# Kernel optimization log

Measured on AMD Instinct MI355X. Metric: run time of the kernel, lower is better.

The kernel has to match this reference:

```python
import jax, jax.numpy as jnp
import numpy as np

B, S, D, H, DH = 2, 2048, 1024, 16, 64
EPS = 1e-6


def setup_inputs() -> dict:
    key = jax.random.key(0)
    k0, k1, k2 = jax.random.split(key, 3)
    x = jax.random.normal(k0, (B, S, D), dtype=jnp.float32)
    mask = jnp.ones((B, S), dtype=bool)
    # NeoX-style rotary angles: half-dim inverse freqs, duplicated to rot_dim=DH
    inv_freq = 1.0 / (10000.0 ** (jnp.arange(0, DH, 2, dtype=jnp.float32) / DH))  # [DH/2]
    ang = jnp.arange(S, dtype=jnp.float32)[:, None] * inv_freq[None, :]            # [S, DH/2]
    freqs = jnp.concatenate([ang, ang], axis=-1)                                    # [S, DH]
    W_qkv = jax.random.normal(k1, (3 * D, D), dtype=jnp.float32) * (D ** -0.5)
    W_out = jax.random.normal(k2, (D, D), dtype=jnp.float32) * (D ** -0.5)
    q_gamma = jnp.ones((DH,), jnp.float32)
    q_beta = jnp.zeros((DH,), jnp.float32)
    k_gamma = jnp.ones((DH,), jnp.float32)
    k_beta = jnp.zeros((DH,), jnp.float32)
    return {"x": x, "mask": mask, "freqs": freqs, "W_qkv": W_qkv, "W_out": W_out,
            "q_gamma": q_gamma, "q_beta": q_beta, "k_gamma": k_gamma, "k_beta": k_beta}


def _layernorm(t, g, b):
    mu = t.mean(-1, keepdims=True)
    var = t.var(-1, keepdims=True)
    return (t - mu) * jax.lax.rsqrt(var + EPS) * g + b


def _rotate_half(t):
    t1, t2 = jnp.split(t, 2, axis=-1)
    return jnp.concatenate([-t2, t1], axis=-1)


def reference(x, mask, freqs, W_qkv, W_out, q_gamma, q_beta, k_gamma, k_beta):
    b, s, d = x.shape
    # fused QKV projection + split into heads: b n (h d) -> b h n d
    qkv = x @ W_qkv.T                                   # [b, s, 3d]
    q, k, v = jnp.split(qkv, 3, axis=-1)
    to_heads = lambda t: t.reshape(b, s, H, DH).transpose(0, 2, 1, 3)
    q, k, v = to_heads(q), to_heads(k), to_heads(v)      # [b, h, s, dh]
    # qk layernorm
    q = _layernorm(q, q_gamma, q_beta)
    k = _layernorm(k, k_gamma, k_beta)
    # rotary embedding (fp32 path in the original; inputs already fp32)
    cos = jnp.cos(freqs)[None, None]                      # [1, 1, s, dh]
    sin = jnp.sin(freqs)[None, None]
    q = q * cos + _rotate_half(q) * sin
    k = k * cos + _rotate_half(k) * sin
    # mask construction: key padding mask 'b j -> b 1 1 j' combined with causal
    key_mask = mask[:, None, None, :]                     # [b, 1, 1, s]
    causal = jnp.tril(jnp.ones((s, s), dtype=bool))       # [s, s]
    comb = key_mask & causal[None, None]                  # [b, 1, s, s]
    row_masked = ~comb.any(axis=-1)                       # [b, 1, s]
    comb = comb.at[..., 0].set(comb[..., 0] | row_masked)
    # SDPA
    scale = DH ** -0.5
    scores = jnp.einsum('bhid,bhjd->bhij', q, k) * scale  # [b, h, s, s]
    scores = jnp.where(comb, scores, jnp.finfo(scores.dtype).min)
    attn = jax.nn.softmax(scores, axis=-1)
    out = jnp.einsum('bhij,bhjd->bhid', attn, v)          # [b, h, s, dh]
    out = jnp.where(row_masked[..., None], 0.0, out)
    # merge heads + output projection
    out = out.transpose(0, 2, 1, 3).reshape(b, s, d)
    return out @ W_out.T
```

## Files before the change

### kernel.cpp

```cpp
#include <hip/hip_runtime.h>
#include <hip/hip_bf16.h>
#include <cstdint>

typedef unsigned short u16;
typedef __attribute__((ext_vector_type(8))) short s16x8;
typedef __attribute__((ext_vector_type(4))) float f32x4;
typedef __attribute__((ext_vector_type(16))) float f32x16;
typedef __attribute__((ext_vector_type(4))) unsigned int u32x4;
typedef __attribute__((ext_vector_type(2))) unsigned int u32x2;
typedef __attribute__((ext_vector_type(4))) u16 u16x4;

#define LOG2E 1.44269504088896340736f

__device__ __forceinline__ u16 f2b(float f) {
  union { float f; unsigned u; } v; v.f = f;
  unsigned r = v.u + 0x7FFF + ((v.u >> 16) & 1);
  return (u16)(r >> 16);
}

__device__ __forceinline__ void gload_lds16(const u16* g, u16* l) {
  __builtin_amdgcn_global_load_lds((const __attribute__((address_space(1))) void*)g,
                                   (__attribute__((address_space(3))) void*)l, 16, 0, 0);
}

__global__ void cvt_bf16(const float* __restrict__ in, u16* __restrict__ out, int n) {
  int i = blockIdx.x * blockDim.x + threadIdx.x;
  if (i < n) out[i] = f2b(in[i]);
}

__global__ void trig_tab(const float* __restrict__ f, float* __restrict__ c,
                         float* __restrict__ s, int n) {
  int i = blockIdx.x * blockDim.x + threadIdx.x;
  if (i < n) { c[i] = cosf(f[i]); s[i] = sinf(f[i]); }
}

__global__ __launch_bounds__(256) void gemm_bt(const u16* __restrict__ A, const u16* __restrict__ B,
                                               float* __restrict__ C, int M, int N, int K) {
  __shared__ u16 sA[128 * 64];
  __shared__ u16 sB[128 * 64];
  const int nbn = N >> 7;
  int bx = blockIdx.x % nbn, by = blockIdx.x / nbn;
  int tid = threadIdx.x, w = tid >> 6, lane = tid & 63;
  int wr = (w >> 1) * 64, wc = (w & 1) * 64;
  int lr = lane >> 3, lc = lane & 7;
  f32x4 acc[4][4] = {};
  size_t arow = (size_t)(by * 128) * K;
  size_t brow = (size_t)(bx * 128) * K;
  for (int k0 = 0; k0 < K; k0 += 64) {
    __syncthreads();
    for (int c = 0; c < 4; ++c) {
      int r = w * 32 + c * 8;
      gload_lds16(A + arow + (size_t)(r + lr) * K + k0 + lc * 8, &sA[r * 64]);
      gload_lds16(B + brow + (size_t)(r + lr) * K + k0 + lc * 8, &sB[r * 64]);
    }
    __syncthreads();
    for (int kk = 0; kk < 64; kk += 32) {
      s16x8 af[4], bf[4];
      int ro = lane & 15, ko = kk + (lane >> 4) * 8;
      for (int m = 0; m < 4; ++m) af[m] = *(const s16x8*)&sA[(wr + m * 16 + ro) * 64 + ko];
      for (int n = 0; n < 4; ++n) bf[n] = *(const s16x8*)&sB[(wc + n * 16 + ro) * 64 + ko];
      for (int m = 0; m < 4; ++m)
        for (int n = 0; n < 4; ++n)
          acc[m][n] = __builtin_amdgcn_mfma_f32_16x16x32_bf16(af[m], bf[n], acc[m][n], 0, 0, 0);
    }
  }
  int ro = lane & 15, rg = lane >> 4;
  for (int m = 0; m < 4; ++m)
    for (int n = 0; n < 4; ++n) {
      int row = by * 128 + wr + m * 16 + rg * 4;
      int col = bx * 128 + wc + n * 16 + ro;
      float* cp = C + (size_t)row * N + col;
      for (int r = 0; r < 4; ++r) cp[(size_t)r * N] = acc[m][n][r];
    }
}

__global__ __launch_bounds__(256) void ln_rope(const float* __restrict__ qkv,
    const float* __restrict__ cosT, const float* __restrict__ sinT,
    const float* __restrict__ qg, const float* __restrict__ qb,
    const float* __restrict__ kg, const float* __restrict__ kb,
    u16* __restrict__ qo, u16* __restrict__ ko, u16* __restrict__ vo) {
  int gw = (blockIdx.x * 256 + threadIdx.x) >> 6;
  int lane = threadIdx.x & 63;
  int h = gw & 15, bs = gw >> 4;
  int s = bs & 2047, b = bs >> 11;
  const float* row = qkv + (size_t)bs * 3072;
  float qv = row[h * 64 + lane];
  float kv = row[1024 + h * 64 + lane];
  float vv = row[2048 + h * 64 + lane];

  float s1q = qv, s2q = qv * qv, s1k = kv, s2k = kv * kv;
  for (int off = 1; off < 64; off <<= 1) {
    s1q += __shfl_xor(s1q, off, 64); s2q += __shfl_xor(s2q, off, 64);
    s1k += __shfl_xor(s1k, off, 64); s2k += __shfl_xor(s2k, off, 64);
  }
  float muq = s1q * (1.f / 64.f), varq = s2q * (1.f / 64.f) - muq * muq;
  float muk = s1k * (1.f / 64.f), vark = s2k * (1.f / 64.f) - muk * muk;
  float qn = (qv - muq) * rsqrtf(varq + 1e-6f) * qg[lane] + qb[lane];
  float kn = (kv - muk) * rsqrtf(vark + 1e-6f) * kg[lane] + kb[lane];

  float cs = cosT[s * 64 + lane], sn = sinT[s * 64 + lane];
  float qh = __shfl_xor(qn, 32, 64); qh = (lane < 32) ? -qh : qh;
  float kh = __shfl_xor(kn, 32, 64); kh = (lane < 32) ? -kh : kh;
  float qr = (qn * cs + qh * sn) * 0.125f;
  float kr = kn * cs + kh * sn;

  size_t oidx = ((size_t)((b * 16 + h) * 2048 + s)) * 64 + lane;
  qo[oidx] = f2b(qr); ko[oidx] = f2b(kr); vo[oidx] = f2b(vv);
}

__global__ __launch_bounds__(256) void transpose_v(const u16* __restrict__ vi, u16* __restrict__ vt) {
  __shared__ __align__(16) u16 tile[64][72];
  int bh = blockIdx.x >> 5, st = blockIdx.x & 31;
  int t = threadIdx.x;
  const u16* src = vi + ((size_t)bh * 2048 + st * 64) * 64;
  int r = t & 63, c = (t >> 6) * 16;
  *(s16x8*)&tile[r][c]     = *(const s16x8*)(src + r * 64 + c);
  *(s16x8*)&tile[r][c + 8] = *(const s16x8*)(src + r * 64 + c + 8);
  __syncthreads();
  int dh = t & 63, so = (t >> 6) * 16;
  alignas(16) u16 buf[16];
  #pragma unroll
  for (int j = 0; j < 16; ++j) buf[j] = tile[so + j][dh];
  u16* dst = vt + ((size_t)bh * 64 + dh) * 2048 + st * 64 + so;
  *(s16x8*)dst       = *(const s16x8*)&buf[0];
  *(s16x8*)(dst + 8) = *(const s16x8*)&buf[8];
}

__global__ __launch_bounds__(64) void attn_fwd2(const u16* __restrict__ qp, const u16* __restrict__ kp,
                                                const u16* __restrict__ vtp, u16* __restrict__ op) {
  __shared__ __align__(16) u16 ot[32][72];
  int bid = ((blockIdx.x & 7) << 7) | (blockIdx.x >> 3);
  int bh = bid >> 5, pr = bid & 31;
  int l = threadIdx.x;
  int ql = l & 31, h5 = l >> 5;
  int b = bh >> 4, h = bh & 15;
  const u16* qb = qp + (size_t)bh * 2048 * 64;
  const u16* kb = kp + (size_t)bh * 2048 * 64;
  const u16* vb = vtp + (size_t)bh * 64 * 2048;

  for (int ss = 0; ss < 2; ++ss) {
    int strip = ss ? (63 - pr) : pr;
    int q0 = strip * 32;
    s16x8 qf[4];
    {
      const u16* qr = qb + (size_t)(q0 + ql) * 64 + h5 * 8;
      #pragma unroll
      for (int t = 0; t < 4; ++t) qf[t] = *(const s16x8*)(qr + 16 * t);
    }
    f32x16 o0 = {}, o1 = {};
    float m = -INFINITY, lsum = 0.f;

    for (int kt = 0; kt <= strip; ++kt) {
      const u16* kr = kb + (size_t)(kt * 32 + ql) * 64 + h5 * 8;
      s16x8 kf[4];
      #pragma unroll
      for (int t = 0; t < 4; ++t) kf[t] = *(const s16x8*)(kr + 16 * t);
      const u16* vr = vb + (size_t)ql * 2048 + kt * 32 + h5 * 8;
      s16x8 vf00 = *(const s16x8*)(vr);
      s16x8 vf01 = *(const s16x8*)(vr + 16);
      s16x8 vf10 = *(const s16x8*)(vr + 32 * 2048);
      s16x8 vf11 = *(const s16x8*)(vr + 32 * 2048 + 16);

      f32x16 sc = {};
      #pragma unroll
      for (int t = 0; t < 4; ++t)
        sc = __builtin_amdgcn_mfma_f32_32x32x16_bf16(kf[t], qf[t], sc, 0, 0, 0);

      if (kt == strip) {
        #pragma unroll
        for (int r = 0; r < 16; ++r) {
          int kloc = (r & 3) + 8 * (r >> 2) + 4 * h5;
          sc[r] = (kloc > ql) ? -INFINITY : sc[r];
        }
      }
      float mx = sc[0];
      #pragma unroll
      for (int r = 1; r < 16; ++r) mx = fmaxf(mx, sc[r]);
      mx = fmaxf(mx, __shfl_xor(mx, 32, 64));
      float mn = fmaxf(m, mx);
      float alpha = __builtin_amdgcn_exp2f((m - mn) * LOG2E);
      float rs = 0.f;
      #pragma unroll
      for (int r = 0; r < 16; ++r) {
        float p = __builtin_amdgcn_exp2f((sc[r] - mn) * LOG2E);
        sc[r] = p; rs += p;
      }
      rs += __shfl_xor(rs, 32, 64);
      lsum = lsum * alpha + rs;
      m = mn;
      #pragma unroll
      for (int r = 0; r < 16; ++r) { o0[r] *= alpha; o1[r] *= alpha; }

      unsigned w[8];
      #pragma unroll
      for (int i = 0; i < 8; ++i)
        asm("v_cvt_pk_bf16_f32 %0, %1, %2" : "=v"(w[i]) : "v"(sc[2 * i]), "v"(sc[2 * i + 1]));
      u32x2 r02 = __builtin_amdgcn_permlane32_swap(w[0], w[2], false, false);
      u32x2 r13 = __builtin_amdgcn_permlane32_swap(w[1], w[3], false, false);
      u32x2 r46 = __builtin_amdgcn_permlane32_swap(w[4], w[6], false, false);
      u32x2 r57 = __builtin_amdgcn_permlane32_swap(w[5], w[7], false, false);
      u32x4 t0v = {r02[0], r13[0], r02[1], r13[1]};
      u32x4 t1v = {r46[0], r57[0], r46[1], r57[1]};
      s16x8 pa0 = __builtin_bit_cast(s16x8, t0v);
      s16x8 pa1 = __builtin_bit_cast(s16x8, t1v);

      o0 = __builtin_amdgcn_mfma_f32_32x32x16_bf16(vf00, pa0, o0, 0, 0, 0);
      o0 = __builtin_amdgcn_mfma_f32_32x32x16_bf16(vf01, pa1, o0, 0, 0, 0);
      o1 = __builtin_amdgcn_mfma_f32_32x32x16_bf16(vf10, pa0, o1, 0, 0, 0);
      o1 = __builtin_amdgcn_mfma_f32_32x32x16_bf16(vf11, pa1, o1, 0, 0, 0);
    }

    float invl = 1.f / lsum;
    #pragma unroll
    for (int d = 0; d < 2; ++d) {
      #pragma unroll
      for (int g = 0; g < 4; ++g) {
        const f32x16& o = d ? o1 : o0;
        u16x4 pkv = { f2b(o[g * 4 + 0] * invl), f2b(o[g * 4 + 1] * invl),
                      f2b(o[g * 4 + 2] * invl), f2b(o[g * 4 + 3] * invl) };
        *(u16x4*)&ot[ql][d * 32 + g * 8 + h5 * 4] = pkv;
      }
    }
    __syncthreads();
    {
      int qrow = l >> 1, dh0 = (l & 1) * 32;
      u16* dst = op + ((size_t)(b * 2048 + q0 + qrow)) * 1024 + h * 64 + dh0;
      #pragma unroll
      for (int k = 0; k < 4; ++k)
        *(s16x8*)(dst + 8 * k) = *(const s16x8*)&ot[qrow][dh0 + 8 * k];
    }
    __syncthreads();
  }
}

extern "C" void kernel_launch(void* const* d_in, const int* in_sizes, int n_in,
                              void* d_out, int out_size, void* d_ws, size_t ws_size,
                              hipStream_t stream) {
  const float* x     = (const float*)d_in[0];
  const float* freqs = (const float*)d_in[2];
  const float* Wqkv  = (const float*)d_in[3];
  const float* Wout  = (const float*)d_in[4];
  const float* qg    = (const float*)d_in[5];
  const float* qb    = (const float*)d_in[6];
  const float* kg    = (const float*)d_in[7];
  const float* kb    = (const float*)d_in[8];
  float* out = (float*)d_out;

  u16* xb    = (u16*)d_ws;
  u16* wqkvb = xb + 4194304;
  u16* woutb = wqkvb + 3145728;
  float* cosT = (float*)(woutb + 1048576);
  float* sinT = cosT + 131072;
  float* qkv  = sinT + 131072;
  u16* qo = (u16*)(qkv + 12582912);
  u16* ko = qo + 4194304;
  u16* vo = ko + 4194304;
  u16* ao = vo + 4194304;
  u16* vt = (u16*)qkv;

  cvt_bf16<<<(4194304 + 255) / 256, 256, 0, stream>>>(x, xb, 4194304);
  cvt_bf16<<<(3145728 + 255) / 256, 256, 0, stream>>>(Wqkv, wqkvb, 3145728);
  cvt_bf16<<<(1048576 + 255) / 256, 256, 0, stream>>>(Wout, woutb, 1048576);
  trig_tab<<<(131072 + 255) / 256, 256, 0, stream>>>(freqs, cosT, sinT, 131072);

  gemm_bt<<<(4096 / 128) * (3072 / 128), 256, 0, stream>>>(xb, wqkvb, qkv, 4096, 3072, 1024);
  ln_rope<<<65536 / 4, 256, 0, stream>>>(qkv, cosT, sinT, qg, qb, kg, kb, qo, ko, vo);
  transpose_v<<<32 * 32, 256, 0, stream>>>(vo, vt);
  attn_fwd2<<<32 * 32, 64, 0, stream>>>(qo, ko, vt, ao);
  gemm_bt<<<(4096 / 128) * (1024 / 128), 256, 0, stream>>>(ao, woutb, out, 4096, 1024, 1024);
}
```

Baseline: 273.9 us.

## Split attention strips into separate blocks, double-buffer K loads, skip redundant rescales

The attention kernel now launches one 64-thread block per 32-row query strip, 2048 blocks in total, where before each block handled two paired strips. Block-to-(head, strip) mapping is derived from the XCD index so each XCD works on a fixed set of heads, which should improve L2 reuse of K/V. K fragments for the next tile are prefetched into alternating register sets while the current tile computes. The row-max reduction becomes a tree, and the alpha rescale of the accumulators is skipped when no lane's max increased. The cost is more blocks with smaller, uneven work per block and higher register pressure from the double-buffered K.

```diff
diff --git a/kernel.cpp b/kernel.cpp
--- a/kernel.cpp
+++ b/kernel.cpp
@@ -126,110 +126,130 @@
   *(s16x8*)(dst + 8) = *(const s16x8*)&buf[8];
 }
 
-__global__ __launch_bounds__(64) void attn_fwd2(const u16* __restrict__ qp, const u16* __restrict__ kp,
+#define LDK(R0, R1, R2, R3, KT) do { \
+    const u16* kr_ = kptr + (size_t)((KT) * 32 + ql) * 64 + h5 * 8; \
+    R0 = *(const s16x8*)(kr_);      R1 = *(const s16x8*)(kr_ + 16); \
+    R2 = *(const s16x8*)(kr_ + 32); R3 = *(const s16x8*)(kr_ + 48); \
+  } while (0)
+
+__global__ __launch_bounds__(64) void attn_fwd3(const u16* __restrict__ qp, const u16* __restrict__ kp,
                                                 const u16* __restrict__ vtp, u16* __restrict__ op) {
   __shared__ __align__(16) u16 ot[32][72];
-  int bid = ((blockIdx.x & 7) << 7) | (blockIdx.x >> 3);
-  int bh = bid >> 5, pr = bid & 31;
+  int bid = blockIdx.x;
+  int xcd = bid & 7, rr = bid >> 3, k8 = rr >> 5, cu = rr & 31;
+  int bh = 4 * xcd + (k8 & 3);
+  int strip = (k8 >> 2) ? (63 - cu) : cu;
   int l = threadIdx.x;
   int ql = l & 31, h5 = l >> 5;
   int b = bh >> 4, h = bh & 15;
-  const u16* qb = qp + (size_t)bh * 2048 * 64;
-  const u16* kb = kp + (size_t)bh * 2048 * 64;
-  const u16* vb = vtp + (size_t)bh * 64 * 2048;
-
-  for (int ss = 0; ss < 2; ++ss) {
-    int strip = ss ? (63 - pr) : pr;
-    int q0 = strip * 32;
-    s16x8 qf[4];
-    {
-      const u16* qr = qb + (size_t)(q0 + ql) * 64 + h5 * 8;
+  const u16* qptr = qp + (size_t)bh * 2048 * 64;
+  const u16* kptr = kp + (size_t)bh * 2048 * 64;
+  const u16* vptr = vtp + (size_t)bh * 64 * 2048;
+
+  int q0 = strip * 32;
+  s16x8 qf[4];
+  {
+    const u16* qr = qptr + (size_t)(q0 + ql) * 64 + h5 * 8;
+    #pragma unroll
+    for (int t = 0; t < 4; ++t) qf[t] = *(const s16x8*)(qr + 16 * t);
+  }
+  f32x16 o0 = {}, o1 = {};
+  float m = -INFINITY, lsum = 0.f;
+
+  auto tile = [&](s16x8 k0, s16x8 k1, s16x8 k2, s16x8 k3, int kt) {
+    const u16* vr = vptr + (size_t)ql * 2048 + kt * 32 + h5 * 8;
+    s16x8 v00 = *(const s16x8*)(vr);
+    s16x8 v01 = *(const s16x8*)(vr + 16);
+    s16x8 v10 = *(const s16x8*)(vr + 32 * 2048);
+    s16x8 v11 = *(const s16x8*)(vr + 32 * 2048 + 16);
+
+    f32x16 sc = {};
+    sc = __builtin_amdgcn_mfma_f32_32x32x16_bf16(k0, qf[0], sc, 0, 0, 0);
+    sc = __builtin_amdgcn_mfma_f32_32x32x16_bf16(k1, qf[1], sc, 0, 0, 0);
+    sc = __builtin_amdgcn_mfma_f32_32x32x16_bf16(k2, qf[2], sc, 0, 0, 0);
+    sc = __builtin_amdgcn_mfma_f32_32x32x16_bf16(k3, qf[3], sc, 0, 0, 0);
+
+    if (kt == strip) {
       #pragma unroll
-      for (int t = 0; t < 4; ++t) qf[t] = *(const s16x8*)(qr + 16 * t);
-    }
-    f32x16 o0 = {}, o1 = {};
-    float m = -INFINITY, lsum = 0.f;
-
-    for (int kt = 0; kt <= strip; ++kt) {
-      const u16* kr = kb + (size_t)(kt * 32 + ql) * 64 + h5 * 8;
-      s16x8 kf[4];
-      #pragma unroll
-      for (int t = 0; t < 4; ++t) kf[t] = *(const s16x8*)(kr + 16 * t);
-      const u16* vr = vb + (size_t)ql * 2048 + kt * 32 + h5 * 8;
-      s16x8 vf00 = *(const s16x8*)(vr);
-      s16x8 vf01 = *(const s16x8*)(vr + 16);
-      s16x8 vf10 = *(const s16x8*)(vr + 32 * 2048);
-      s16x8 vf11 = *(const s16x8*)(vr + 32 * 2048 + 16);
-
-      f32x16 sc = {};
-      #pragma unroll
-      for (int t = 0; t < 4; ++t)
-        sc = __builtin_amdgcn_mfma_f32_32x32x16_bf16(kf[t], qf[t], sc, 0, 0, 0);
-
-      if (kt == strip) {
-        #pragma unroll
-        for (int r = 0; r < 16; ++r) {
-          int kloc = (r & 3) + 8 * (r >> 2) + 4 * h5;
-          sc[r] = (kloc > ql) ? -INFINITY : sc[r];
-        }
+      for (int r = 0; r < 16; ++r) {
+        int kloc = (r & 3) + 8 * (r >> 2) + 4 * h5;
+        sc[r] = (kloc > ql) ? -INFINITY : sc[r];
       }
-      float mx = sc[0];
-      #pragma unroll
-      for (int r = 1; r < 16; ++r) mx = fmaxf(mx, sc[r]);
-      mx = fmaxf(mx, __shfl_xor(mx, 32, 64));
+    }
+    float t8[8], t4[4];
+    #pragma unroll
+    for (int i = 0; i < 8; ++i) t8[i] = fmaxf(sc[2 * i], sc[2 * i + 1]);
+    #pragma unroll
+    for (int i = 0; i < 4; ++i) t4[i] = fmaxf(t8[2 * i], t8[2 * i + 1]);
+    float mx = fmaxf(fmaxf(t4[0], t4[1]), fmaxf(t4[2], t4[3]));
+    mx = fmaxf(mx, __shfl_xor(mx, 32, 64));
+
+    if (__any(mx > m)) {
       float mn = fmaxf(m, mx);
       float alpha = __builtin_amdgcn_exp2f((m - mn) * LOG2E);
-      float rs = 0.f;
-      #pragma unroll
-      for (int r = 0; r < 16; ++r) {
-        float p = __builtin_amdgcn_exp2f((sc[r] - mn) * LOG2E);
-        sc[r] = p; rs += p;
-      }
-      rs += __shfl_xor(rs, 32, 64);
-      lsum = lsum * alpha + rs;
-      m = mn;
       #pragma unroll
       for (int r = 0; r < 16; ++r) { o0[r] *= alpha; o1[r] *= alpha; }
-
-      unsigned w[8];
-      #pragma unroll
-      for (int i = 0; i < 8; ++i)
-        asm("v_cvt_pk_bf16_f32 %0, %1, %2" : "=v"(w[i]) : "v"(sc[2 * i]), "v"(sc[2 * i + 1]));
-      u32x2 r02 = __builtin_amdgcn_permlane32_swap(w[0], w[2], false, false);
-      u32x2 r13 = __builtin_amdgcn_permlane32_swap(w[1], w[3], false, false);
-      u32x2 r46 = __builtin_amdgcn_permlane32_swap(w[4], w[6], false, false);
-      u32x2 r57 = __builtin_amdgcn_permlane32_swap(w[5], w[7], false, false);
-      u32x4 t0v = {r02[0], r13[0], r02[1], r13[1]};
-      u32x4 t1v = {r46[0], r57[0], r46[1], r57[1]};
-      s16x8 pa0 = __builtin_bit_cast(s16x8, t0v);
-      s16x8 pa1 = __builtin_bit_cast(s16x8, t1v);
-
-      o0 = __builtin_amdgcn_mfma_f32_32x32x16_bf16(vf00, pa0, o0, 0, 0, 0);
-      o0 = __builtin_amdgcn_mfma_f32_32x32x16_bf16(vf01, pa1, o0, 0, 0, 0);
-      o1 = __builtin_amdgcn_mfma_f32_32x32x16_bf16(vf10, pa0, o1, 0, 0, 0);
-      o1 = __builtin_amdgcn_mfma_f32_32x32x16_bf16(vf11, pa1, o1, 0, 0, 0);
-    }
-
-    float invl = 1.f / lsum;
-    #pragma unroll
-    for (int d = 0; d < 2; ++d) {
-      #pragma unroll
-      for (int g = 0; g < 4; ++g) {
-        const f32x16& o = d ? o1 : o0;
-        u16x4 pkv = { f2b(o[g * 4 + 0] * invl), f2b(o[g * 4 + 1] * invl),
-                      f2b(o[g * 4 + 2] * invl), f2b(o[g * 4 + 3] * invl) };
-        *(u16x4*)&ot[ql][d * 32 + g * 8 + h5 * 4] = pkv;
-      }
-    }
-    __syncthreads();
-    {
-      int qrow = l >> 1, dh0 = (l & 1) * 32;
-      u16* dst = op + ((size_t)(b * 2048 + q0 + qrow)) * 1024 + h * 64 + dh0;
-      #pragma unroll
-      for (int k = 0; k < 4; ++k)
-        *(s16x8*)(dst + 8 * k) = *(const s16x8*)&ot[qrow][dh0 + 8 * k];
-    }
-    __syncthreads();
+      lsum *= alpha;
+      m = mn;
+    }
+    float rs = 0.f;
+    #pragma unroll
+    for (int r = 0; r < 16; ++r) {
+      float p = __builtin_amdgcn_exp2f((sc[r] - m) * LOG2E);
+      sc[r] = p; rs += p;
+    }
+    rs += __shfl_xor(rs, 32, 64);
+    lsum += rs;
+
+    unsigned w[8];
+    #pragma unroll
+    for (int i = 0; i < 8; ++i)
+      asm("v_cvt_pk_bf16_f32 %0, %1, %2" : "=v"(w[i]) : "v"(sc[2 * i]), "v"(sc[2 * i + 1]));
+    u32x2 r02 = __builtin_amdgcn_permlane32_swap(w[0], w[2], false, false);
+    u32x2 r13 = __builtin_amdgcn_permlane32_swap(w[1], w[3], false, false);
+    u32x2 r46 = __builtin_amdgcn_permlane32_swap(w[4], w[6], false, false);
+    u32x2 r57 = __builtin_amdgcn_permlane32_swap(w[5], w[7], false, false);
+    u32x4 t0v = {r02[0], r13[0], r02[1], r13[1]};
+    u32x4 t1v = {r46[0], r57[0], r46[1], r57[1]};
+    s16x8 pa0 = __builtin_bit_cast(s16x8, t0v);
+    s16x8 pa1 = __builtin_bit_cast(s16x8, t1v);
+
+    o0 = __builtin_amdgcn_mfma_f32_32x32x16_bf16(v00, pa0, o0, 0, 0, 0);
+    o0 = __builtin_amdgcn_mfma_f32_32x32x16_bf16(v01, pa1, o0, 0, 0, 0);
+    o1 = __builtin_amdgcn_mfma_f32_32x32x16_bf16(v10, pa0, o1, 0, 0, 0);
+    o1 = __builtin_amdgcn_mfma_f32_32x32x16_bf16(v11, pa1, o1, 0, 0, 0);
+  };
+
+  s16x8 a0, a1, a2, a3, c0, c1, c2, c3;
+  LDK(a0, a1, a2, a3, 0);
+  int kt = 0;
+  for (;;) {
+    if (kt + 1 <= strip) LDK(c0, c1, c2, c3, kt + 1);
+    tile(a0, a1, a2, a3, kt);
+    if (++kt > strip) break;
+    if (kt + 1 <= strip) LDK(a0, a1, a2, a3, kt + 1);
+    tile(c0, c1, c2, c3, kt);
+    if (++kt > strip) break;
+  }
+
+  float invl = 1.f / lsum;
+  #pragma unroll
+  for (int d = 0; d < 2; ++d) {
+    #pragma unroll
+    for (int g = 0; g < 4; ++g) {
+      const f32x16& o = d ? o1 : o0;
+      u16x4 pkv = { f2b(o[g * 4 + 0] * invl), f2b(o[g * 4 + 1] * invl),
+                    f2b(o[g * 4 + 2] * invl), f2b(o[g * 4 + 3] * invl) };
+      *(u16x4*)&ot[ql][d * 32 + g * 8 + h5 * 4] = pkv;
+    }
+  }
+  __syncthreads();
+  {
+    int qrow = l >> 1, dh0 = (l & 1) * 32;
+    u16* dst = op + ((size_t)(b * 2048 + q0 + qrow)) * 1024 + h * 64 + dh0;
+    #pragma unroll
+    for (int kk = 0; kk < 4; ++kk)
+      *(s16x8*)(dst + 8 * kk) = *(const s16x8*)&ot[qrow][dh0 + 8 * kk];
   }
 }
 
@@ -266,6 +286,6 @@
   gemm_bt<<<(4096 / 128) * (3072 / 128), 256, 0, stream>>>(xb, wqkvb, qkv, 4096, 3072, 1024);
   ln_rope<<<65536 / 4, 256, 0, stream>>>(qkv, cosT, sinT, qg, qb, kg, kb, qo, ko, vo);
   transpose_v<<<32 * 32, 256, 0, stream>>>(vo, vt);
-  attn_fwd2<<<32 * 32, 64, 0, stream>>>(qo, ko, vt, ao);
+  attn_fwd3<<<2048, 64, 0, stream>>>(qo, ko, vt, ao);
   gemm_bt<<<(4096 / 128) * (1024 / 128), 256, 0, stream>>>(ao, woutb, out, 4096, 1024, 1024);
 }
```

Result: no change. 269.4 us (-1.6%).
